# Optimization experiments

Measured on AMD Instinct MI355X. Metric: run time of the kernel, lower is better.

The kernel has to match this reference:

```python
import jax, jax.numpy as jnp
import numpy as np

EMBED_DIM = 512
NUM_HEADS = 16
TGT_LEN = 1024
BSZ = 4
HEAD_DIM = EMBED_DIM // NUM_HEADS


def setup_inputs() -> dict:
    key = jax.random.key(0)
    ks = jax.random.split(key, 12)
    E = EMBED_DIM
    s = 1.0 / np.sqrt(E)
    query = jax.random.normal(ks[0], (TGT_LEN, BSZ, E), dtype=jnp.float32)
    attn_bias = jax.random.normal(ks[1], (BSZ * NUM_HEADS, TGT_LEN, TGT_LEN), dtype=jnp.float32)
    key_padding_mask = jax.random.randint(ks[2], (BSZ, TGT_LEN), 0, 2) == 1
    q_w = jax.random.normal(ks[3], (E, E), dtype=jnp.float32) * s
    q_b = jax.random.normal(ks[4], (E,), dtype=jnp.float32) * 0.02
    k_w = jax.random.normal(ks[5], (E, E), dtype=jnp.float32) * s
    k_b = jax.random.normal(ks[6], (E,), dtype=jnp.float32) * 0.02
    v_w = jax.random.normal(ks[7], (E, E), dtype=jnp.float32) * s
    v_b = jax.random.normal(ks[8], (E,), dtype=jnp.float32) * 0.02
    out_w = jax.random.normal(ks[9], (E, E), dtype=jnp.float32) * s
    out_b = jax.random.normal(ks[10], (E,), dtype=jnp.float32) * 0.02
    return {
        "query": query, "attn_bias": attn_bias, "key_padding_mask": key_padding_mask,
        "q_w": q_w, "q_b": q_b, "k_w": k_w, "k_b": k_b,
        "v_w": v_w, "v_b": v_b, "out_w": out_w, "out_b": out_b,
    }


def reference(query, attn_bias, key_padding_mask, q_w, q_b, k_w, k_b, v_w, v_b, out_w, out_b):
    Tlen, B, E = query.shape
    H, hd = NUM_HEADS, HEAD_DIM
    scaling = hd ** -0.5
    # self-attention: q/k/v all from query (Linear uses y = x @ W.T + b)
    q = (query @ q_w.T + q_b) * scaling
    k = query @ k_w.T + k_b
    v = query @ v_w.T + v_b
    # [T, B, E] -> [B*H, T, hd]
    q = q.reshape(Tlen, B * H, hd).transpose(1, 0, 2)
    k = k.reshape(Tlen, B * H, hd).transpose(1, 0, 2)
    v = v.reshape(Tlen, B * H, hd).transpose(1, 0, 2)
    # scores [B*H, T, S]
    aw = jnp.einsum('bth,bsh->bts', q, k) + attn_bias
    # key padding mask: [B, S] -> broadcast over heads and tgt
    aw = aw.reshape(B, H, Tlen, Tlen)
    aw = jnp.where(key_padding_mask[:, None, None, :], -jnp.inf, aw)
    aw = aw.reshape(B * H, Tlen, Tlen)
    probs = jax.nn.softmax(aw.astype(jnp.float32), axis=-1)
    attn = jnp.einsum('bts,bsh->bth', probs.astype(query.dtype), v)
    attn = attn.transpose(1, 0, 2).reshape(Tlen, B, E)
    out = attn @ out_w.T + out_b
    # need_weights=True, need_head_weights=False -> mean over heads, [B, T, S]
    attn_weights_avg = probs.reshape(B, H, Tlen, Tlen).mean(axis=1)
    return out, attn_weights_avg
```

## Files before the change

kernel.cpp:

```cpp
#include <hip/hip_runtime.h>
#include <math.h>

typedef __bf16 bf16x8 __attribute__((ext_vector_type(8)));
typedef __bf16 bf16x4 __attribute__((ext_vector_type(4)));
typedef float  f32x4  __attribute__((ext_vector_type(4)));

__global__ __launch_bounds__(256)
void cvt_w(const float* __restrict__ w0, const float* __restrict__ w1,
           const float* __restrict__ w2, const float* __restrict__ w3,
           __bf16* __restrict__ d0, __bf16* __restrict__ d1,
           __bf16* __restrict__ d2, __bf16* __restrict__ d3)
{
    const int y = blockIdx.y;
    const float* s = (y == 0) ? w0 : (y == 1) ? w1 : (y == 2) ? w2 : w3;
    __bf16*      d = (y == 0) ? d0 : (y == 1) ? d1 : (y == 2) ? d2 : d3;
    const int i = blockIdx.x * 256 + threadIdx.x;
    float4 a = *(const float4*)(s + (size_t)i * 8);
    float4 b = *(const float4*)(s + (size_t)i * 8 + 4);
    bf16x8 v;
    v[0] = (__bf16)a.x; v[1] = (__bf16)a.y; v[2] = (__bf16)a.z; v[3] = (__bf16)a.w;
    v[4] = (__bf16)b.x; v[5] = (__bf16)b.y; v[6] = (__bf16)b.z; v[7] = (__bf16)b.w;
    *(bf16x8*)(d + (size_t)i * 8) = v;
}

__global__ __launch_bounds__(256, 2)
void qkv_proj(const float* __restrict__ X,
              const __bf16* __restrict__ Wqb, const __bf16* __restrict__ Wkb,
              const __bf16* __restrict__ Wvb,
              const float* __restrict__ bq, const float* __restrict__ bk,
              const float* __restrict__ bv,
              __bf16* __restrict__ qTb, __bf16* __restrict__ kTb,
              __bf16* __restrict__ vTb)
{
    const int tid  = threadIdx.x;
    const int w    = tid >> 6;
    const int lane = tid & 63;
    const int lq   = lane & 15;
    const int quad = lane >> 4;
    const int n0    = blockIdx.x * 64 + (w >> 1) * 32;
    const int obase = blockIdx.y * 128 + (w & 1) * 64;

    const __bf16* const Wz[3] = { Wqb, Wkb, Wvb };

    f32x4 acc[3][2][4] = {};
    for (int k0 = 0; k0 < 512; k0 += 32) {
        bf16x8 af[2];
#pragma unroll
        for (int m = 0; m < 2; m++) {
            const float* xp = X + (size_t)(n0 + m * 16 + lq) * 512 + k0 + quad * 8;
            float4 x0 = *(const float4*)xp;
            float4 x1 = *(const float4*)(xp + 4);
            bf16x8 v;
            v[0] = (__bf16)x0.x; v[1] = (__bf16)x0.y; v[2] = (__bf16)x0.z; v[3] = (__bf16)x0.w;
            v[4] = (__bf16)x1.x; v[5] = (__bf16)x1.y; v[6] = (__bf16)x1.z; v[7] = (__bf16)x1.w;
            af[m] = v;
        }
#pragma unroll
        for (int z = 0; z < 3; z++) {
            bf16x8 bfr[4];
#pragma unroll
            for (int nn = 0; nn < 4; nn++)
                bfr[nn] = *(const bf16x8*)(Wz[z] + (size_t)(obase + nn * 16 + lq) * 512 + k0 + quad * 8);
#pragma unroll
            for (int m = 0; m < 2; m++)
#pragma unroll
                for (int nn = 0; nn < 4; nn++)
                    acc[z][m][nn] = __builtin_amdgcn_mfma_f32_16x16x32_bf16(af[m], bfr[nn], acc[z][m][nn], 0, 0, 0);
        }
    }

    const float* const ba[3] = { bq, bk, bv };
    const float scaling = 0.17677669529663687f;
#pragma unroll
    for (int z = 0; z < 3; z++)
#pragma unroll
        for (int m = 0; m < 2; m++)
#pragma unroll
            for (int nn = 0; nn < 4; nn++)
#pragma unroll
                for (int r = 0; r < 4; r++) {
                    const int n = n0 + m * 16 + quad * 4 + r;
                    const int o = obase + nn * 16 + lq;
                    float val = acc[z][m][nn][r] + ba[z][o];
                    const int t = n >> 2, b = n & 3;
                    const int h = o >> 5, d = o & 31;
                    const int bh = b * 16 + h;
                    if (z == 0)
                        qTb[(((size_t)bh * 1024 + t) << 5) + d] = (__bf16)(val * scaling);
                    else if (z == 1)
                        kTb[(((size_t)bh * 1024 + t) << 5) + d] = (__bf16)val;
                    else
                        vTb[(((size_t)bh * 32 + d) << 10) + t] = (__bf16)val;
                }
}

__global__ __launch_bounds__(256)
void out_proj(const __bf16* __restrict__ A, const __bf16* __restrict__ Wb,
              const float* __restrict__ bias, float* __restrict__ out)
{
    const int tid  = threadIdx.x;
    const int w    = tid >> 6;
    const int lane = tid & 63;
    const int lq   = lane & 15;
    const int quad = lane >> 4;
    const int n0    = blockIdx.x * 64 + (w >> 1) * 32;
    const int obase = blockIdx.y * 128 + (w & 1) * 64;

    f32x4 acc[2][4] = {};
    for (int k0 = 0; k0 < 512; k0 += 32) {
        bf16x8 af[2], bfr[4];
#pragma unroll
        for (int m = 0; m < 2; m++)
            af[m] = *(const bf16x8*)(A + (size_t)(n0 + m * 16 + lq) * 512 + k0 + quad * 8);
#pragma unroll
        for (int nn = 0; nn < 4; nn++)
            bfr[nn] = *(const bf16x8*)(Wb + (size_t)(obase + nn * 16 + lq) * 512 + k0 + quad * 8);
#pragma unroll
        for (int m = 0; m < 2; m++)
#pragma unroll
            for (int nn = 0; nn < 4; nn++)
                acc[m][nn] = __builtin_amdgcn_mfma_f32_16x16x32_bf16(af[m], bfr[nn], acc[m][nn], 0, 0, 0);
    }
#pragma unroll
    for (int m = 0; m < 2; m++)
#pragma unroll
        for (int nn = 0; nn < 4; nn++)
#pragma unroll
            for (int r = 0; r < 4; r++) {
                const int n = n0 + m * 16 + quad * 4 + r;
                const int o = obase + nn * 16 + lq;
                out[(size_t)n * 512 + o] = acc[m][nn][r] + bias[o];
            }
}

__global__ __launch_bounds__(512, 2)
void attn_mfma(const __bf16* __restrict__ qTb, const __bf16* __restrict__ kTb,
               const __bf16* __restrict__ vTb, const float* __restrict__ bias,
               const int* __restrict__ mask, __bf16* __restrict__ attnb,
               float* __restrict__ avgf)
{
    __shared__ float smem[17408];
    float* const Op0  = smem;
    float* const red0 = &smem[8448];
    __bf16* const Pbase = (__bf16*)&smem[8704];

    const int tid  = threadIdx.x;
    const int w    = tid >> 6;
    const int lane = tid & 63;
    const int lq   = lane & 15;
    const int quad = lane >> 4;

    const int bid = blockIdx.y * 64 + blockIdx.x;
    const int nb  = (bid & 7) * 32 + (bid >> 3);
    const int t0  = (nb & 63) * 16;
    const int b   = nb >> 6;
    const int sbase = w * 128;

    __bf16* const Pw = Pbase + w * 2176;

    unsigned mbits = 0;
    {
        const int* mp = mask + b * 1024 + sbase + quad * 4;
#pragma unroll
        for (int j = 0; j < 8; j++) {
            int4 m4 = *(const int4*)(mp + j * 16);
            mbits |= (unsigned)(m4.x != 0) << (j * 4 + 0);
            mbits |= (unsigned)(m4.y != 0) << (j * 4 + 1);
            mbits |= (unsigned)(m4.z != 0) << (j * 4 + 2);
            mbits |= (unsigned)(m4.w != 0) << (j * 4 + 3);
        }
    }

    const float* const bb = bias + (((size_t)(b * 16)) << 20) +
                            (((size_t)(t0 + lq)) << 10) + sbase + quad * 4;
    const __bf16* const qp0 = qTb + (((size_t)(b * 16) * 1024 + t0) << 5) +
                              lq * 32 + quad * 8;

    bf16x8 qa = *(const bf16x8*)qp0;
    f32x4 cj[8];
#pragma unroll
    for (int j = 0; j < 8; j++) cj[j] = *(const f32x4*)(bb + j * 16);

    float avg_reg[32] = {};

    for (int hh = 0; hh < 16; hh++) {
        const int bh = b * 16 + hh;
        float* const Op  = Op0  + (hh & 1) * 4224;
        float* const red = red0 + (hh & 1) * 128;
        const __bf16* kp = kTb + ((size_t)bh << 15);
        const __bf16* vp = vTb + ((size_t)bh << 15);

        f32x4 acc[8];
#pragma unroll
        for (int j = 0; j < 8; j++) {
            bf16x8 kb = *(const bf16x8*)(kp + (size_t)(sbase + j * 16 + lq) * 32 + quad * 8);
            acc[j] = __builtin_amdgcn_mfma_f32_16x16x32_bf16(kb, qa, cj[j], 0, 0, 0);
        }

        bf16x8 v0r[4], v1r[4];
#pragma unroll
        for (int ks = 0; ks < 4; ks++) {
            v0r[ks] = *(const bf16x8*)(vp + (size_t)lq * 1024 + sbase + ks * 32 + quad * 8);
            v1r[ks] = *(const bf16x8*)(vp + (size_t)(16 + lq) * 1024 + sbase + ks * 32 + quad * 8);
        }

        __builtin_amdgcn_sched_barrier(0);

        if (hh < 15) {
            qa = *(const bf16x8*)(qp0 + ((size_t)(hh + 1) << 15));
            const float* bn = bb + ((size_t)(hh + 1) << 20);
#pragma unroll
            for (int j = 0; j < 8; j++) cj[j] = *(const f32x4*)(bn + j * 16);
        }

        float sm = 0.f;
#pragma unroll
        for (int j = 0; j < 8; j++)
#pragma unroll
            for (int r = 0; r < 4; r++) {
                float p = __expf(acc[j][r]);
                p = ((mbits >> (j * 4 + r)) & 1u) ? 0.f : p;
                acc[j][r] = p;
                sm += p;
            }
        sm += __shfl_xor(sm, 16);
        sm += __shfl_xor(sm, 32);

#pragma unroll
        for (int j = 0; j < 8; j++) {
            bf16x4 pv;
            pv[0] = (__bf16)acc[j][0]; pv[1] = (__bf16)acc[j][1];
            pv[2] = (__bf16)acc[j][2]; pv[3] = (__bf16)acc[j][3];
            *(bf16x4*)&Pw[lq * 136 + j * 16 + quad * 4] = pv;
        }
        if (lane < 16) red[w * 16 + lane] = sm;

        f32x4 o0 = {0.f, 0.f, 0.f, 0.f}, o1 = {0.f, 0.f, 0.f, 0.f};
#pragma unroll
        for (int ks = 0; ks < 4; ks++) {
            bf16x8 pa = *(const bf16x8*)&Pw[lq * 136 + ks * 32 + quad * 8];
            o0 = __builtin_amdgcn_mfma_f32_16x16x32_bf16(pa, v0r[ks], o0, 0, 0, 0);
            o1 = __builtin_amdgcn_mfma_f32_16x16x32_bf16(pa, v1r[ks], o1, 0, 0, 0);
        }
#pragma unroll
        for (int r = 0; r < 4; r++) {
            Op[w * 528 + (quad * 4 + r) * 33 + lq]      = o0[r];
            Op[w * 528 + (quad * 4 + r) * 33 + 16 + lq] = o1[r];
        }

        __builtin_amdgcn_sched_barrier(0);
        asm volatile("s_waitcnt lgkmcnt(0)" ::: "memory");
        __builtin_amdgcn_s_barrier();
        __builtin_amdgcn_sched_barrier(0);

        {
            const int t = tid >> 5, d = tid & 31;
            float s = 0.f, o = 0.f;
#pragma unroll
            for (int w2 = 0; w2 < 8; w2++) s += red[w2 * 16 + t];
#pragma unroll
            for (int w2 = 0; w2 < 8; w2++) o += Op[w2 * 528 + t * 33 + d];
            attnb[((size_t)(t0 + t) * 4 + b) * 512 + hh * 32 + d] = (__bf16)(o / s);
        }

        float s_all = 0.f;
#pragma unroll
        for (int w2 = 0; w2 < 8; w2++) s_all += red[w2 * 16 + lq];
        const float inv = 1.0f / s_all;
#pragma unroll
        for (int j = 0; j < 8; j++)
#pragma unroll
            for (int r = 0; r < 4; r++)
                avg_reg[j * 4 + r] += acc[j][r] * inv;
    }

    float* ap = avgf + ((size_t)(b * 1024 + t0 + lq) << 10) + sbase + quad * 4;
#pragma unroll
    for (int j = 0; j < 8; j++) {
        f32x4 v = { avg_reg[j * 4 + 0] * 0.0625f, avg_reg[j * 4 + 1] * 0.0625f,
                    avg_reg[j * 4 + 2] * 0.0625f, avg_reg[j * 4 + 3] * 0.0625f };
        *(f32x4*)(ap + j * 16) = v;
    }
}

extern "C" void kernel_launch(void* const* d_in, const int* in_sizes, int n_in,
                              void* d_out, int out_size, void* d_ws, size_t ws_size,
                              hipStream_t stream)
{
    const float* query     = (const float*)d_in[0];
    const float* attn_bias = (const float*)d_in[1];
    const int*   mask      = (const int*)d_in[2];
    const float* q_w       = (const float*)d_in[3];
    const float* q_b       = (const float*)d_in[4];
    const float* k_w       = (const float*)d_in[5];
    const float* k_b       = (const float*)d_in[6];
    const float* v_w       = (const float*)d_in[7];
    const float* v_b       = (const float*)d_in[8];
    const float* out_w     = (const float*)d_in[9];
    const float* out_b     = (const float*)d_in[10];

    float* out     = (float*)d_out;
    float* avg_out = out + (size_t)2097152;

    char* wsb = (char*)d_ws;
    __bf16* Wqb   = (__bf16*)(wsb);
    __bf16* Wkb   = (__bf16*)(wsb + ((size_t)512 << 10));
    __bf16* Wvb   = (__bf16*)(wsb + ((size_t)1 << 20));
    __bf16* Wob   = (__bf16*)(wsb + ((size_t)1 << 20) + ((size_t)512 << 10));
    __bf16* qTb   = (__bf16*)(wsb + ((size_t)2  << 20));
    __bf16* kTb   = (__bf16*)(wsb + ((size_t)6  << 20));
    __bf16* vTb   = (__bf16*)(wsb + ((size_t)10 << 20));
    __bf16* attnb = (__bf16*)(wsb + ((size_t)14 << 20));

    cvt_w<<<dim3(128, 4), dim3(256), 0, stream>>>(
        q_w, k_w, v_w, out_w, Wqb, Wkb, Wvb, Wob);

    qkv_proj<<<dim3(64, 4), dim3(256), 0, stream>>>(
        query, Wqb, Wkb, Wvb, q_b, k_b, v_b, qTb, kTb, vTb);

    attn_mfma<<<dim3(64, 4), dim3(512), 0, stream>>>(
        qTb, kTb, vTb, attn_bias, mask, attnb, avg_out);

    out_proj<<<dim3(64, 4), dim3(256), 0, stream>>>(attnb, Wob, out_b, out);
}
```

Before: 149.4 us.

## Stream attention bias through LDS with async global_load_lds double buffering

The attention kernel now prefetches the next head's fp32 bias tile into a double-buffered, XOR-swizzled LDS region using global_load_lds, instead of loading it into registers. A per-head barrier with a partial vmcnt wait is added so the transfer overlaps the current head's compute. The P, partial-output and row-sum scratch areas are merged into one per-wave swizzled region. Separately, the QKV and output projection grids are doubled with narrower 64-column output tiles to raise parallelism. The larger LDS footprint (160KB) and the extra barrier per head may limit occupancy.

Result: slower. 163.7 us (+9.6%).

```diff
diff --git a/kernel.cpp b/kernel.cpp
--- a/kernel.cpp
+++ b/kernel.cpp
@@ -4,6 +4,13 @@
 typedef __bf16 bf16x8 __attribute__((ext_vector_type(8)));
 typedef __bf16 bf16x4 __attribute__((ext_vector_type(4)));
 typedef float  f32x4  __attribute__((ext_vector_type(4)));
+
+__device__ __forceinline__ void gload16(const float* g, float* l)
+{
+    __builtin_amdgcn_global_load_lds(
+        (const __attribute__((address_space(1))) void*)g,
+        (__attribute__((address_space(3))) void*)l, 16, 0, 0);
+}
 
 __global__ __launch_bounds__(256)
 void cvt_w(const float* __restrict__ w0, const float* __restrict__ w1,
@@ -38,11 +45,11 @@
     const int lq   = lane & 15;
     const int quad = lane >> 4;
     const int n0    = blockIdx.x * 64 + (w >> 1) * 32;
-    const int obase = blockIdx.y * 128 + (w & 1) * 64;
+    const int obase = blockIdx.y * 64 + (w & 1) * 32;
 
     const __bf16* const Wz[3] = { Wqb, Wkb, Wvb };
 
-    f32x4 acc[3][2][4] = {};
+    f32x4 acc[3][2][2] = {};
     for (int k0 = 0; k0 < 512; k0 += 32) {
         bf16x8 af[2];
 #pragma unroll
@@ -57,14 +64,14 @@
         }
 #pragma unroll
         for (int z = 0; z < 3; z++) {
-            bf16x8 bfr[4];
-#pragma unroll
-            for (int nn = 0; nn < 4; nn++)
+            bf16x8 bfr[2];
+#pragma unroll
+            for (int nn = 0; nn < 2; nn++)
                 bfr[nn] = *(const bf16x8*)(Wz[z] + (size_t)(obase + nn * 16 + lq) * 512 + k0 + quad * 8);
 #pragma unroll
             for (int m = 0; m < 2; m++)
 #pragma unroll
-                for (int nn = 0; nn < 4; nn++)
+                for (int nn = 0; nn < 2; nn++)
                     acc[z][m][nn] = __builtin_amdgcn_mfma_f32_16x16x32_bf16(af[m], bfr[nn], acc[z][m][nn], 0, 0, 0);
         }
     }
@@ -76,7 +83,7 @@
 #pragma unroll
         for (int m = 0; m < 2; m++)
 #pragma unroll
-            for (int nn = 0; nn < 4; nn++)
+            for (int nn = 0; nn < 2; nn++)
 #pragma unroll
                 for (int r = 0; r < 4; r++) {
                     const int n = n0 + m * 16 + quad * 4 + r;
@@ -94,7 +101,7 @@
                 }
 }
 
-__global__ __launch_bounds__(256)
+__global__ __launch_bounds__(256, 2)
 void out_proj(const __bf16* __restrict__ A, const __bf16* __restrict__ Wb,
               const float* __restrict__ bias, float* __restrict__ out)
 {
@@ -104,27 +111,27 @@
     const int lq   = lane & 15;
     const int quad = lane >> 4;
     const int n0    = blockIdx.x * 64 + (w >> 1) * 32;
-    const int obase = blockIdx.y * 128 + (w & 1) * 64;
-
-    f32x4 acc[2][4] = {};
+    const int obase = blockIdx.y * 64 + (w & 1) * 32;
+
+    f32x4 acc[2][2] = {};
     for (int k0 = 0; k0 < 512; k0 += 32) {
-        bf16x8 af[2], bfr[4];
+        bf16x8 af[2], bfr[2];
 #pragma unroll
         for (int m = 0; m < 2; m++)
             af[m] = *(const bf16x8*)(A + (size_t)(n0 + m * 16 + lq) * 512 + k0 + quad * 8);
 #pragma unroll
-        for (int nn = 0; nn < 4; nn++)
+        for (int nn = 0; nn < 2; nn++)
             bfr[nn] = *(const bf16x8*)(Wb + (size_t)(obase + nn * 16 + lq) * 512 + k0 + quad * 8);
 #pragma unroll
         for (int m = 0; m < 2; m++)
 #pragma unroll
-            for (int nn = 0; nn < 4; nn++)
+            for (int nn = 0; nn < 2; nn++)
                 acc[m][nn] = __builtin_amdgcn_mfma_f32_16x16x32_bf16(af[m], bfr[nn], acc[m][nn], 0, 0, 0);
     }
 #pragma unroll
     for (int m = 0; m < 2; m++)
 #pragma unroll
-        for (int nn = 0; nn < 4; nn++)
+        for (int nn = 0; nn < 2; nn++)
 #pragma unroll
             for (int r = 0; r < 4; r++) {
                 const int n = n0 + m * 16 + quad * 4 + r;
@@ -133,16 +140,13 @@
             }
 }
 
-__global__ __launch_bounds__(512, 2)
+__global__ __attribute__((amdgpu_waves_per_eu(2, 2))) __launch_bounds__(512)
 void attn_mfma(const __bf16* __restrict__ qTb, const __bf16* __restrict__ kTb,
                const __bf16* __restrict__ vTb, const float* __restrict__ bias,
                const int* __restrict__ mask, __bf16* __restrict__ attnb,
                float* __restrict__ avgf)
 {
-    __shared__ float smem[17408];
-    float* const Op0  = smem;
-    float* const red0 = &smem[8448];
-    __bf16* const Pbase = (__bf16*)&smem[8704];
+    __shared__ float smem[40960];
 
     const int tid  = threadIdx.x;
     const int w    = tid >> 6;
@@ -155,8 +159,6 @@
     const int t0  = (nb & 63) * 16;
     const int b   = nb >> 6;
     const int sbase = w * 128;
-
-    __bf16* const Pw = Pbase + w * 2176;
 
     unsigned mbits = 0;
     {
@@ -171,47 +173,68 @@
         }
     }
 
-    const float* const bb = bias + (((size_t)(b * 16)) << 20) +
-                            (((size_t)(t0 + lq)) << 10) + sbase + quad * 4;
     const __bf16* const qp0 = qTb + (((size_t)(b * 16) * 1024 + t0) << 5) +
                               lq * 32 + quad * 8;
+    const __bf16* const kp0 = kTb + ((size_t)(b * 16) << 15);
+    const __bf16* const vp0 = vTb + ((size_t)(b * 16) << 15);
+    const float*  const bias0 = bias + (((size_t)(b * 16)) << 20) + (size_t)t0 * 1024;
 
     bf16x8 qa = *(const bf16x8*)qp0;
-    f32x4 cj[8];
-#pragma unroll
-    for (int j = 0; j < 8; j++) cj[j] = *(const f32x4*)(bb + j * 16);
+#pragma unroll
+    for (int c = 0; c < 8; c++) {
+        const int row = 2 * w + (c >> 2), qtr = c & 3;
+        const int g   = (qtr * 64 + lane) ^ ((row & 7) << 1);
+        gload16(bias0 + (size_t)row * 1024 + g * 4, &smem[row * 1024 + qtr * 256]);
+    }
+    __syncthreads();
 
     float avg_reg[32] = {};
+    float* const Xw = &smem[32768 + w * 1024];
+    __bf16* const Pw = (__bf16*)Xw;
+    const int psw = (lq & 7) << 3;
+    const int csw = (lq & 7) << 1;
 
     for (int hh = 0; hh < 16; hh++) {
-        const int bh = b * 16 + hh;
-        float* const Op  = Op0  + (hh & 1) * 4224;
-        float* const red = red0 + (hh & 1) * 128;
-        const __bf16* kp = kTb + ((size_t)bh << 15);
-        const __bf16* vp = vTb + ((size_t)bh << 15);
-
-        f32x4 acc[8];
-#pragma unroll
-        for (int j = 0; j < 8; j++) {
-            bf16x8 kb = *(const bf16x8*)(kp + (size_t)(sbase + j * 16 + lq) * 32 + quad * 8);
-            acc[j] = __builtin_amdgcn_mfma_f32_16x16x32_bf16(kb, qa, cj[j], 0, 0, 0);
-        }
-
+        const int cur = hh & 1;
+        const __bf16* kp = kp0 + ((size_t)hh << 15);
+        const __bf16* vp = vp0 + ((size_t)hh << 15);
+
+        bf16x8 kb[8];
+#pragma unroll
+        for (int j = 0; j < 8; j++)
+            kb[j] = *(const bf16x8*)(kp + (size_t)(sbase + j * 16 + lq) * 32 + quad * 8);
         bf16x8 v0r[4], v1r[4];
 #pragma unroll
         for (int ks = 0; ks < 4; ks++) {
             v0r[ks] = *(const bf16x8*)(vp + (size_t)lq * 1024 + sbase + ks * 32 + quad * 8);
             v1r[ks] = *(const bf16x8*)(vp + (size_t)(16 + lq) * 1024 + sbase + ks * 32 + quad * 8);
         }
-
-        __builtin_amdgcn_sched_barrier(0);
-
+        __builtin_amdgcn_sched_barrier(0);
+
+        bf16x8 qan = qa;
         if (hh < 15) {
-            qa = *(const bf16x8*)(qp0 + ((size_t)(hh + 1) << 15));
-            const float* bn = bb + ((size_t)(hh + 1) << 20);
-#pragma unroll
-            for (int j = 0; j < 8; j++) cj[j] = *(const f32x4*)(bn + j * 16);
-        }
+            const float* bsrc = bias0 + ((size_t)(hh + 1) << 20);
+            float* ldst = &smem[(cur ^ 1) * 16384];
+#pragma unroll
+            for (int c = 0; c < 8; c++) {
+                const int row = 2 * w + (c >> 2), qtr = c & 3;
+                const int g   = (qtr * 64 + lane) ^ ((row & 7) << 1);
+                gload16(bsrc + (size_t)row * 1024 + g * 4, ldst + row * 1024 + qtr * 256);
+            }
+            qan = *(const bf16x8*)(qp0 + ((size_t)(hh + 1) << 15));
+        }
+        __builtin_amdgcn_sched_barrier(0);
+
+        f32x4 acc[8];
+        const float* cbase = &smem[cur * 16384 + lq * 1024];
+#pragma unroll
+        for (int j = 0; j < 8; j++) {
+            const int g = w * 32 + j * 4 + quad;
+            f32x4 cjv = *(const f32x4*)(cbase + ((g ^ csw) << 2));
+            acc[j] = __builtin_amdgcn_mfma_f32_16x16x32_bf16(kb[j], qa, cjv, 0, 0, 0);
+        }
+        qa = qan;
+        __builtin_amdgcn_sched_barrier(0);
 
         float sm = 0.f;
 #pragma unroll
@@ -231,22 +254,23 @@
             bf16x4 pv;
             pv[0] = (__bf16)acc[j][0]; pv[1] = (__bf16)acc[j][1];
             pv[2] = (__bf16)acc[j][2]; pv[3] = (__bf16)acc[j][3];
-            *(bf16x4*)&Pw[lq * 136 + j * 16 + quad * 4] = pv;
-        }
-        if (lane < 16) red[w * 16 + lane] = sm;
+            *(bf16x4*)&Pw[lq * 128 + ((j * 16 + quad * 4) ^ psw)] = pv;
+        }
 
         f32x4 o0 = {0.f, 0.f, 0.f, 0.f}, o1 = {0.f, 0.f, 0.f, 0.f};
 #pragma unroll
         for (int ks = 0; ks < 4; ks++) {
-            bf16x8 pa = *(const bf16x8*)&Pw[lq * 136 + ks * 32 + quad * 8];
+            bf16x8 pa = *(const bf16x8*)&Pw[lq * 128 + ((ks * 32 + quad * 8) ^ psw)];
             o0 = __builtin_amdgcn_mfma_f32_16x16x32_bf16(pa, v0r[ks], o0, 0, 0, 0);
             o1 = __builtin_amdgcn_mfma_f32_16x16x32_bf16(pa, v1r[ks], o1, 0, 0, 0);
         }
+
 #pragma unroll
         for (int r = 0; r < 4; r++) {
-            Op[w * 528 + (quad * 4 + r) * 33 + lq]      = o0[r];
-            Op[w * 528 + (quad * 4 + r) * 33 + 16 + lq] = o1[r];
-        }
+            Xw[(quad * 4 + r) * 33 + lq]      = o0[r];
+            Xw[(quad * 4 + r) * 33 + 16 + lq] = o1[r];
+        }
+        if (lane < 16) Xw[544 + lane] = sm;
 
         __builtin_amdgcn_sched_barrier(0);
         asm volatile("s_waitcnt lgkmcnt(0)" ::: "memory");
@@ -257,21 +281,27 @@
             const int t = tid >> 5, d = tid & 31;
             float s = 0.f, o = 0.f;
 #pragma unroll
-            for (int w2 = 0; w2 < 8; w2++) s += red[w2 * 16 + t];
-#pragma unroll
-            for (int w2 = 0; w2 < 8; w2++) o += Op[w2 * 528 + t * 33 + d];
+            for (int w2 = 0; w2 < 8; w2++) s += smem[32768 + w2 * 1024 + 544 + t];
+#pragma unroll
+            for (int w2 = 0; w2 < 8; w2++) o += smem[32768 + w2 * 1024 + t * 33 + d];
             attnb[((size_t)(t0 + t) * 4 + b) * 512 + hh * 32 + d] = (__bf16)(o / s);
         }
 
         float s_all = 0.f;
 #pragma unroll
-        for (int w2 = 0; w2 < 8; w2++) s_all += red[w2 * 16 + lq];
+        for (int w2 = 0; w2 < 8; w2++) s_all += smem[32768 + w2 * 1024 + 544 + lq];
         const float inv = 1.0f / s_all;
 #pragma unroll
         for (int j = 0; j < 8; j++)
 #pragma unroll
             for (int r = 0; r < 4; r++)
                 avg_reg[j * 4 + r] += acc[j][r] * inv;
+
+        __builtin_amdgcn_sched_barrier(0);
+        asm volatile("s_waitcnt vmcnt(1) lgkmcnt(0)" ::: "memory");
+        __builtin_amdgcn_sched_barrier(0);
+        __builtin_amdgcn_s_barrier();
+        __builtin_amdgcn_sched_barrier(0);
     }
 
     float* ap = avgf + ((size_t)(b * 1024 + t0 + lq) << 10) + sbase + quad * 4;
@@ -315,11 +345,11 @@
     cvt_w<<<dim3(128, 4), dim3(256), 0, stream>>>(
         q_w, k_w, v_w, out_w, Wqb, Wkb, Wvb, Wob);
 
-    qkv_proj<<<dim3(64, 4), dim3(256), 0, stream>>>(
+    qkv_proj<<<dim3(64, 8), dim3(256), 0, stream>>>(
         query, Wqb, Wkb, Wvb, q_b, k_b, v_b, qTb, kTb, vTb);
 
     attn_mfma<<<dim3(64, 4), dim3(512), 0, stream>>>(
         qTb, kTb, vTb, attn_bias, mask, attnb, avg_out);
 
-    out_proj<<<dim3(64, 4), dim3(256), 0, stream>>>(attnb, Wob, out_b, out);
-}
+    out_proj<<<dim3(64, 8), dim3(256), 0, stream>>>(attnb, Wob, out_b, out);
+}
```

## Software-pipeline K fragments and attention bias two heads ahead in attn kernel

Applied to the files above, without the earlier changes.

Restructures the per-head loop into a two-stage ping-pong so that K fragments are prefetched one head ahead and attention-bias tiles two heads ahead, in alternating register sets. The goal is to hide global-load latency for K and the large fp32 bias stream behind the softmax and PV work of the current head. It also switches the occupancy hint to amdgpu_waves_per_eu(2,2) and enlarges the shared-memory array, though no new code uses the extra space. The cost is much higher register pressure (two K and two bias buffers) and wrap-around loads on the last iterations that fetch unused data.

Result: slower. 211.6 us (+41.7%).

```diff
diff --git a/kernel.cpp b/kernel.cpp
--- a/kernel.cpp
+++ b/kernel.cpp
@@ -133,13 +133,13 @@
             }
 }
 
-__global__ __launch_bounds__(512, 2)
+__global__ __attribute__((amdgpu_waves_per_eu(2, 2))) __launch_bounds__(512)
 void attn_mfma(const __bf16* __restrict__ qTb, const __bf16* __restrict__ kTb,
                const __bf16* __restrict__ vTb, const float* __restrict__ bias,
                const int* __restrict__ mask, __bf16* __restrict__ attnb,
                float* __restrict__ avgf)
 {
-    __shared__ float smem[17408];
+    __shared__ float smem[20800];
     float* const Op0  = smem;
     float* const red0 = &smem[8448];
     __bf16* const Pbase = (__bf16*)&smem[8704];
@@ -175,27 +175,26 @@
                             (((size_t)(t0 + lq)) << 10) + sbase + quad * 4;
     const __bf16* const qp0 = qTb + (((size_t)(b * 16) * 1024 + t0) << 5) +
                               lq * 32 + quad * 8;
+    const __bf16* const kp0 = kTb + ((size_t)(b * 16) << 15);
+    const __bf16* const vp0 = vTb + ((size_t)(b * 16) << 15);
 
     bf16x8 qa = *(const bf16x8*)qp0;
-    f32x4 cj[8];
-#pragma unroll
-    for (int j = 0; j < 8; j++) cj[j] = *(const f32x4*)(bb + j * 16);
+    bf16x8 kbA[8], kbB[8];
+#pragma unroll
+    for (int j = 0; j < 8; j++)
+        kbA[j] = *(const bf16x8*)(kp0 + (size_t)(sbase + j * 16 + lq) * 32 + quad * 8);
+    f32x4 cjA[8], cjB[8];
+#pragma unroll
+    for (int j = 0; j < 8; j++) cjA[j] = *(const f32x4*)(bb + j * 16);
+#pragma unroll
+    for (int j = 0; j < 8; j++) cjB[j] = *(const f32x4*)(bb + (1ull << 20) + j * 16);
 
     float avg_reg[32] = {};
 
-    for (int hh = 0; hh < 16; hh++) {
-        const int bh = b * 16 + hh;
+    auto body = [&](bf16x8 (&kbC)[8], bf16x8 (&kbN)[8], f32x4 (&cjC)[8], int hh) {
         float* const Op  = Op0  + (hh & 1) * 4224;
         float* const red = red0 + (hh & 1) * 128;
-        const __bf16* kp = kTb + ((size_t)bh << 15);
-        const __bf16* vp = vTb + ((size_t)bh << 15);
-
-        f32x4 acc[8];
-#pragma unroll
-        for (int j = 0; j < 8; j++) {
-            bf16x8 kb = *(const bf16x8*)(kp + (size_t)(sbase + j * 16 + lq) * 32 + quad * 8);
-            acc[j] = __builtin_amdgcn_mfma_f32_16x16x32_bf16(kb, qa, cj[j], 0, 0, 0);
-        }
+        const __bf16* vp = vp0 + ((size_t)hh << 15);
 
         bf16x8 v0r[4], v1r[4];
 #pragma unroll
@@ -203,15 +202,27 @@
             v0r[ks] = *(const bf16x8*)(vp + (size_t)lq * 1024 + sbase + ks * 32 + quad * 8);
             v1r[ks] = *(const bf16x8*)(vp + (size_t)(16 + lq) * 1024 + sbase + ks * 32 + quad * 8);
         }
-
-        __builtin_amdgcn_sched_barrier(0);
-
-        if (hh < 15) {
-            qa = *(const bf16x8*)(qp0 + ((size_t)(hh + 1) << 15));
-            const float* bn = bb + ((size_t)(hh + 1) << 20);
-#pragma unroll
-            for (int j = 0; j < 8; j++) cj[j] = *(const f32x4*)(bn + j * 16);
-        }
+        __builtin_amdgcn_sched_barrier(0);
+
+        f32x4 acc[8];
+#pragma unroll
+        for (int j = 0; j < 8; j++)
+            acc[j] = __builtin_amdgcn_mfma_f32_16x16x32_bf16(kbC[j], qa, cjC[j], 0, 0, 0);
+        __builtin_amdgcn_sched_barrier(0);
+
+        {
+            const int h1 = (hh + 1) & 15;
+            const int h2 = (hh + 2) & 15;
+            qa = *(const bf16x8*)(qp0 + ((size_t)h1 << 15));
+            const __bf16* kpn = kp0 + ((size_t)h1 << 15);
+#pragma unroll
+            for (int j = 0; j < 8; j++)
+                kbN[j] = *(const bf16x8*)(kpn + (size_t)(sbase + j * 16 + lq) * 32 + quad * 8);
+            const float* bn = bb + ((size_t)h2 << 20);
+#pragma unroll
+            for (int j = 0; j < 8; j++) cjC[j] = *(const f32x4*)(bn + j * 16);
+        }
+        __builtin_amdgcn_sched_barrier(0);
 
         float sm = 0.f;
 #pragma unroll
@@ -272,6 +283,11 @@
 #pragma unroll
             for (int r = 0; r < 4; r++)
                 avg_reg[j * 4 + r] += acc[j][r] * inv;
+    };
+
+    for (int hp = 0; hp < 8; hp++) {
+        body(kbA, kbB, cjA, hp * 2);
+        body(kbB, kbA, cjB, hp * 2 + 1);
     }
 
     float* ap = avgf + ((size_t)(b * 1024 + t0 + lq) << 10) + sbase + quad * 4;
```
